# Optimization experiments

Hardware: AMD Instinct MI355X
Metric: run time of the kernel (lower is better)

Reference implementation:

```python
import jax, jax.numpy as jnp
import numpy as np

MAX_GAP = 32  # n_index = 2*MAX_GAP+1 = 65


def setup_inputs() -> dict:
    key = jax.random.key(0)
    kW, kb = jax.random.split(key)
    B, S, E, N = 1, 1024, 128, 2 * MAX_GAP + 1
    idxs = jnp.arange(B * S, dtype=jnp.int64 if jax.config.jax_enable_x64 else jnp.int32).reshape(B, S)
    W = jax.random.normal(kW, (E, N), dtype=jnp.float32)  # nn.Linear weight (out, in)
    b = jax.random.normal(kb, (E,), dtype=jnp.float32)    # nn.Linear bias
    return {"idxs": idxs, "W": W, "b": b}


def reference(idxs, W, b):
    # pos_2d[b,i,j] = clip(idxs[b,j] - idxs[b,i], -max_gap, max_gap) + max_gap  in [0, n_index)
    pos = jnp.clip(idxs[:, None, :] - idxs[:, :, None], -MAX_GAP, MAX_GAP) + MAX_GAP  # (B,S,S)
    # onehot(pos) @ W.T + b  ==  row-gather from W.T plus bias (same math, no dense one-hot)
    return jnp.take(W.T, pos, axis=0) + b  # (B,S,S,E)
```

## Files before the change

### kernel.cpp

```cpp
#include <hip/hip_runtime.h>


#define MAXGAP 32
#define NIDX   65
#define EDIM   128
#define E4     32
#define PADE   132
#define CHUNKS 2

typedef float f32x4 __attribute__((ext_vector_type(4)));

__global__ __launch_bounds__(256) void relpos2d_kernel(
    const int* __restrict__ idxs,
    const float* __restrict__ W,
    const float* __restrict__ bias,
    f32x4* __restrict__ out,
    int S, int halfS)
{
    __shared__ float table[NIDX * PADE];
    __shared__ int   jidx[512];

    for (int t = threadIdx.x; t < NIDX * EDIM; t += 256) {
        float w = W[t];
        int e = t / NIDX;
        int p = t - e * NIDX;
        table[p * PADE + e] = w + bias[e];
    }

    const int i     = blockIdx.x >> 1;
    const int chunk = blockIdx.x & (CHUNKS - 1);
    const int jbase = chunk * halfS;

    for (int t = threadIdx.x; t < halfS; t += 256)
        jidx[t] = idxs[jbase + t];

    __syncthreads();

    const int lane4 = threadIdx.x & 31;
    const int jsub  = threadIdx.x >> 5;
    const int idx_i = idxs[i];

    f32x4* __restrict__ orow = out + (size_t)i * S * E4 + (size_t)jbase * E4;

    #pragma unroll 4
    for (int jj = 0; jj < halfS; jj += 8) {
        int j = jj + jsub;
        int d = jidx[j] - idx_i;
        d = d < -MAXGAP ? -MAXGAP : (d > MAXGAP ? MAXGAP : d);
        int p = d + MAXGAP;

        f32x4 v = reinterpret_cast<const f32x4*>(&table[p * PADE])[lane4];
        orow[(size_t)j * E4 + lane4] = v;
    }
}

extern "C" void kernel_launch(void* const* d_in, const int* in_sizes, int n_in,
                              void* d_out, int out_size, void* d_ws, size_t ws_size,
                              hipStream_t stream) {
    const int*   idxs = (const int*)  d_in[0];
    const float* W    = (const float*)d_in[1];
    const float* bias = (const float*)d_in[2];

    f32x4* out = (f32x4*)d_out;

    const int S     = in_sizes[0];
    const int halfS = S / 2;
    const int grid  = S * CHUNKS;

    relpos2d_kernel<<<grid, 256, 0, stream>>>(idxs, W, bias, out, S, halfS);
}
```

Baseline: 96.96 us.

## Precompute biased lookup table in workspace and stream output from global reads

Adds a small kernel that builds the transposed W+bias table once in workspace memory. The main kernel then reads rows from that global table, which should stay cache-resident, and no longer rebuilds a 33KB LDS table in each of the 2048 blocks. The intent is to remove the per-block table construction and the LDS footprint that limits occupancy. In exchange it adds a second launch and relies on L2 hits for the gathers. The old LDS kernel is kept as a fallback when the workspace is too small.

```diff
diff --git a/kernel.cpp b/kernel.cpp
--- a/kernel.cpp
+++ b/kernel.cpp
@@ -10,7 +10,49 @@
 
 typedef float f32x4 __attribute__((ext_vector_type(4)));
 
-__global__ __launch_bounds__(256) void relpos2d_kernel(
+__global__ __launch_bounds__(256) void build_table_kernel(
+    const float* __restrict__ W, const float* __restrict__ bias,
+    float* __restrict__ tbl)
+{
+    int t = blockIdx.x * 256 + threadIdx.x;
+    if (t < NIDX * EDIM) {
+        float w = W[t];
+        int e = t / NIDX;
+        int p = t - e * NIDX;
+        tbl[p * EDIM + e] = w + bias[e];
+    }
+}
+
+__global__ __launch_bounds__(256, 8) void relpos2d_stream_kernel(
+    const int* __restrict__ idxs,
+    const f32x4* __restrict__ tbl4,
+    f32x4* __restrict__ out,
+    int S, int halfS)
+{
+    const int i     = blockIdx.x >> 1;
+    const int chunk = blockIdx.x & (CHUNKS - 1);
+    const int jbase = chunk * halfS;
+
+    const int lane4 = threadIdx.x & 31;
+    const int jsub  = threadIdx.x >> 5;
+    const int idx_i = idxs[i];
+
+    const int* __restrict__ jptr = idxs + jbase;
+    f32x4* __restrict__ orow = out + (size_t)i * S * E4 + (size_t)jbase * E4;
+
+    #pragma unroll 4
+    for (int jj = 0; jj < halfS; jj += 8) {
+        int j = jj + jsub;
+        int d = jptr[j] - idx_i;
+        d = d < -MAXGAP ? -MAXGAP : (d > MAXGAP ? MAXGAP : d);
+        int p = d + MAXGAP;
+
+        f32x4 v = tbl4[p * E4 + lane4];
+        orow[(size_t)j * E4 + lane4] = v;
+    }
+}
+
+__global__ __launch_bounds__(256) void relpos2d_lds_kernel(
     const int* __restrict__ idxs,
     const float* __restrict__ W,
     const float* __restrict__ bias,
@@ -67,5 +109,14 @@
     const int halfS = S / 2;
     const int grid  = S * CHUNKS;
 
-    relpos2d_kernel<<<grid, 256, 0, stream>>>(idxs, W, bias, out, S, halfS);
+    const size_t tbl_bytes = (size_t)NIDX * EDIM * sizeof(float);
+
+    if (ws_size >= tbl_bytes) {
+        float* tbl = (float*)d_ws;
+        build_table_kernel<<<(NIDX * EDIM + 255) / 256, 256, 0, stream>>>(W, bias, tbl);
+        relpos2d_stream_kernel<<<grid, 256, 0, stream>>>(
+            idxs, (const f32x4*)tbl, out, S, halfS);
+    } else {
+        relpos2d_lds_kernel<<<grid, 256, 0, stream>>>(idxs, W, bias, out, S, halfS);
+    }
 }
```

After: 106.6 us. +10.0%, slower.
